# Performance work log

Hardware: AMD Instinct MI355X
Metric: run time of the kernel (lower is better)

## Reference

```python
import jax, jax.numpy as jnp
import numpy as np

N_CLASS = 85
BLANK = N_CLASS - 1  # blank_index = n_class - 1
ALPHA = 0.05
B, T, D = 4096, 96, 64


def setup_inputs() -> dict:
    key = jax.random.key(0)
    k1, k2, k3, k4 = jax.random.split(key, 4)
    preds = jax.random.normal(k1, (B, T, N_CLASS), dtype=jnp.float32)
    features = jax.random.normal(k2, (B, T, D), dtype=jnp.float32)
    labels = jax.random.randint(k3, (B, T), 0, N_CLASS, dtype=jnp.int32)
    centers = jax.random.normal(k4, (N_CLASS, D), dtype=jnp.float32) * 0.01
    return {"preds": preds, "features": features, "labels": labels, "centers": centers}


def _char_mask(pred_labels):
    # CTC collapse: keep non-blank positions that are the last of a repeat run.
    is_char = pred_labels != BLANK
    rep = pred_labels[:, :-1] == pred_labels[:, 1:]          # [B, T-1]
    tail = pred_labels[:, :1] > BLANK                         # always False (as in source)
    char_rep = jnp.concatenate([rep, tail], axis=1)           # [B, T]
    return is_char & jnp.logical_not(char_rep)


def reference(preds, features, labels, centers):
    # preds:    [B, T, n_class] softmax/logits -> argmax decode
    # features: [B, T, feat_dims]
    # labels:   [B, T] int, char label aligned to each timestep
    pred_labels = jnp.argmax(preds, axis=-1)                  # [B, T]
    mask = _char_mask(pred_labels).astype(features.dtype)     # [B, T] ragged-as-mask

    centers_batch = centers[labels]                           # gather -> [B, T, D]
    diff = centers_batch - features                           # [B, T, D]

    # tf.nn.l2_loss = sum(x^2)/2, restricted to valid char positions
    loss = 0.5 * jnp.sum(mask * jnp.sum(diff * diff, axis=-1))

    # unique_with_counts analog: per-class counts of valid char positions
    labels_flat = labels.reshape(-1)
    mask_flat = mask.reshape(-1)
    counts = jax.ops.segment_sum(mask_flat, labels_flat, num_segments=N_CLASS)  # [n_class]
    appear = counts[labels]                                   # [B, T]

    # alpha * diff / (1 + appear_times), zeroed outside char positions
    delta = ALPHA * diff * (mask / (1.0 + appear))[..., None]  # [B, T, D]

    # scatter_nd: centers.assign_sub(scatter of per-char deltas)
    upd = jax.ops.segment_sum(delta.reshape(-1, D), labels_flat, num_segments=N_CLASS)
    new_centers = centers - upd                               # [n_class, D]
    return loss, new_centers
```

## Files before the change

kernel.cpp:

```cpp
#include <hip/hip_runtime.h>
#include <cstdint>

#define BB     4096
#define TT     96
#define NC     85
#define BLANKC 84
#define DD     64
#define ALPHA  0.05f
#define BT     (BB * TT)
#define SLICE_F (NC * 17)
#define NF4    (TT * NC / 4)
#define RPBA   4
#define NBA    (BB / RPBA)
#define NBM    512

__global__ __launch_bounds__(512) void k_amask(const float4* __restrict__ p4,
                                               const int* __restrict__ labels,
                                               unsigned* __restrict__ labm,
                                               int* __restrict__ hpartT,
                                               float* __restrict__ out) {
    __shared__ float rows[8][12 * NC];
    __shared__ int   pls[RPBA * TT + 1];
    __shared__ int   h[NC];
    int tid  = threadIdx.x;
    int blk  = blockIdx.x;
    int lane = tid & 63;
    int w    = tid >> 6;
    if (tid < NC) h[tid] = 0;
    if (blk == 0 && tid == 480) out[0] = 0.f;
    int labreg = (tid < RPBA * TT) ? labels[blk * RPBA * TT + tid] : 0;

    const float4* src = p4 + (size_t)(blk * RPBA) * NF4 + 255 * w;
    float4 v0 = src[lane];
    float4 v1 = src[lane + 64];
    float4 v2 = src[lane + 128];
    float4 v3 = src[min(lane + 192, 254)];

    const int c0t[4] = {0, 22, 43, 64};
    const int c1t[4] = {22, 43, 64, 85};

    for (int i = 0; i < RPBA; ++i) {
        float4* dst = (float4*)rows[w];
        dst[lane]       = v0;
        dst[lane + 64]  = v1;
        dst[lane + 128] = v2;
        if (lane < 63) dst[lane + 192] = v3;
        if (i + 1 < RPBA) {
            const float4* s2 = p4 + (size_t)(blk * RPBA + i + 1) * NF4 + 255 * w;
            v0 = s2[lane];
            v1 = s2[lane + 64];
            v2 = s2[lane + 128];
            v3 = s2[min(lane + 192, 254)];
        }
        int r = lane >> 2, q = lane & 3;
        float bv = -3.4e38f; int bc = 127;
        if (lane < 48) {
            const float* row = rows[w] + r * NC;
            int c0 = c0t[q], c1 = c1t[q];
            bv = row[c0]; bc = c0;
            for (int c = c0 + 1; c < c1; ++c) {
                float v = row[c];
                if (v > bv) { bv = v; bc = c; }
            }
        }
#pragma unroll
        for (int m = 1; m <= 2; m <<= 1) {
            float ov = __shfl_xor(bv, m);
            int   oc = __shfl_xor(bc, m);
            if (ov > bv || (ov == bv && oc < bc)) { bv = ov; bc = oc; }
        }
        if (lane < 48 && (lane & 3) == 0) pls[i * TT + w * 12 + r] = bc;
    }
    __syncthreads();
    if (tid < RPBA * TT) {
        int p  = pls[tid];
        int lp = tid % TT;
        int m  = (p != BLANKC) && (lp == TT - 1 || p != pls[tid + 1]);
        labm[blk * RPBA * TT + tid] = (unsigned)labreg | ((unsigned)m << 31);
        atomicAdd(&h[labreg], m);
    }
    __syncthreads();
    if (tid < NC) hpartT[tid * NBA + blk] = h[tid];
}

__global__ __launch_bounds__(512, 6) void k_main(const float* __restrict__ feat,
                                                 const unsigned* __restrict__ labm,
                                                 float* __restrict__ updp,
                                                 float* __restrict__ lossp) {
    __shared__ float sl[8 * SLICE_F];
    __shared__ float lred[8];
    int tid = threadIdx.x;
    for (int i = tid; i < 8 * SLICE_F; i += 512) sl[i] = 0.f;
    __syncthreads();

    int lane = tid & 63;
    int w    = tid >> 6;
    int dq   = w & 3;
    int wg   = w >> 2;
    int sub  = lane >> 4;
    int l16  = lane & 15;
    float* slice = sl + w * SLICE_F;

    const int ppc = BT / (NBM * 2);
    const int nss = ppc / 16;
    int p0  = (blockIdx.x * 2 + wg) * ppc;
    const float* fbase = feat + dq * 16 + l16;

    float lsum = 0.f;
    float fA0, fA1, fA2, fA3, fB0, fB1, fB2, fB3;
    uint4 lA0, lA1, lA2, lA3, lB0, lB1, lB2, lB3;

#define ISSUE(P, f0, f1, f2, f3, q0, q1, q2, q3) do {            \
    int _p = (P);                                                \
    q0 = *(const uint4*)(labm + _p);                             \
    q1 = *(const uint4*)(labm + _p + 4);                         \
    q2 = *(const uint4*)(labm + _p + 8);                         \
    q3 = *(const uint4*)(labm + _p + 12);                        \
    f0 = fbase[(size_t)(_p + sub) * DD];                         \
    f1 = fbase[(size_t)(_p + 4 + sub) * DD];                     \
    f2 = fbase[(size_t)(_p + 8 + sub) * DD];                     \
    f3 = fbase[(size_t)(_p + 12 + sub) * DD];                    \
} while (0)

#define SUBSTEP(lv, fc) do {                                     \
    unsigned a0 = lv.x & 0x7fffffffu, a1 = lv.y & 0x7fffffffu,   \
             a2 = lv.z & 0x7fffffffu, a3 = lv.w & 0x7fffffffu;   \
    bool dup = (a0 == a1) | (a0 == a2) | (a0 == a3) |            \
               (a1 == a2) | (a1 == a3) | (a2 == a3);             \
    unsigned lw = (sub & 2) ? ((sub & 1) ? lv.w : lv.z)          \
                            : ((sub & 1) ? lv.y : lv.x);         \
    float m = (float)(lw >> 31);                                 \
    int  la = (int)(lw & 0x7fffffffu);                           \
    float c = m * (fc);                                          \
    lsum = fmaf(c, (fc), lsum);                                  \
    int a = la * 17 + l16;                                       \
    if (!dup) slice[a] += c;                                     \
    else      atomicAdd(&slice[a], c);                           \
} while (0)

    ISSUE(p0, fA0, fA1, fA2, fA3, lA0, lA1, lA2, lA3);
    for (int ss = 0; ss < nss; ss += 2) {
        if (ss + 1 < nss)
            ISSUE(p0 + (ss + 1) * 16, fB0, fB1, fB2, fB3, lB0, lB1, lB2, lB3);
        SUBSTEP(lA0, fA0); SUBSTEP(lA1, fA1);
        SUBSTEP(lA2, fA2); SUBSTEP(lA3, fA3);
        if (ss + 1 < nss) {
            if (ss + 2 < nss)
                ISSUE(p0 + (ss + 2) * 16, fA0, fA1, fA2, fA3, lA0, lA1, lA2, lA3);
            SUBSTEP(lB0, fB0); SUBSTEP(lB1, fB1);
            SUBSTEP(lB2, fB2); SUBSTEP(lB3, fB3);
        }
    }
#undef ISSUE
#undef SUBSTEP
    __syncthreads();

    float* myp = updp + (size_t)blockIdx.x * (NC * DD);
    for (int i = tid; i < NC * DD; i += 512) {
        int r = i >> 6, d = i & 63;
        int qq = d >> 4, d16 = d & 15;
        myp[i] = sl[qq * SLICE_F + r * 17 + d16] +
                 sl[(qq + 4) * SLICE_F + r * 17 + d16];
    }
#pragma unroll
    for (int off = 32; off; off >>= 1) lsum += __shfl_xor(lsum, off);
    if (lane == 0) lred[w] = lsum;
    __syncthreads();
    if (tid == 0) {
        float s = 0.f;
#pragma unroll
        for (int ww = 0; ww < 8; ++ww) s += lred[ww];
        lossp[blockIdx.x] = s;
    }
}

__global__ __launch_bounds__(256) void k_reduce(const float* __restrict__ updp,
                                                const float* __restrict__ lossp,
                                                const float* __restrict__ centers,
                                                const int* __restrict__ hpartT,
                                                float* __restrict__ out) {
    __shared__ float sred[256];
    __shared__ float sr[4];
    __shared__ int   scnt;
    int tid = threadIdx.x;
    int bid = blockIdx.x;
    if (bid < NC * 4) {
        int j = bid >> 2, q = bid & 3;
        int cs = 0;
        for (int t = tid; t < NBA; t += 256) cs += hpartT[j * NBA + t];
#pragma unroll
        for (int off = 32; off; off >>= 1) cs += __shfl_xor(cs, off);
        int lane = tid & 63, wv = tid >> 6;
        if (lane == 0) ((int*)sred)[wv] = cs;
        __syncthreads();
        if (tid == 0)
            scnt = ((int*)sred)[0] + ((int*)sred)[1] +
                   ((int*)sred)[2] + ((int*)sred)[3];
        __syncthreads();
        float cnt = (float)scnt;
        int i = tid & 15;
        int c16 = tid >> 4;
        const int per = NBM >> 4;
        int col = j * DD + q * 16 + i;
        float s = 0.f;
        for (int b = c16 * per; b < (c16 + 1) * per; ++b)
            s += updp[(size_t)b * (NC * DD) + col];
        sred[tid] = s;
        __syncthreads();
        if (tid < 16) {
            float F = 0.f;
#pragma unroll
            for (int cc = 0; cc < 16; ++cc) F += sred[cc * 16 + i];
            float c   = centers[col];
            float scale = ALPHA / (1.f + cnt);
            out[1 + col] = c - scale * (cnt * c - F);
            float lp = cnt * c * c - 2.f * c * F;
#pragma unroll
            for (int off = 8; off; off >>= 1) lp += __shfl_xor(lp, off);
            if (i == 0) atomicAdd(&out[0], 0.5f * lp);
        }
    } else {
        float s = 0.f;
        for (int t = tid; t < NBM; t += 256) s += lossp[t];
#pragma unroll
        for (int off = 32; off; off >>= 1) s += __shfl_xor(s, off);
        int lane = tid & 63, wv = tid >> 6;
        if (lane == 0) sr[wv] = s;
        __syncthreads();
        if (tid == 0) atomicAdd(&out[0], 0.5f * (sr[0] + sr[1] + sr[2] + sr[3]));
    }
}

extern "C" void kernel_launch(void* const* d_in, const int* in_sizes, int n_in,
                              void* d_out, int out_size, void* d_ws, size_t ws_size,
                              hipStream_t stream) {
    const float* preds    = (const float*)d_in[0];
    const float* features = (const float*)d_in[1];
    const int*   labels   = (const int*)d_in[2];
    const float* centers  = (const float*)d_in[3];
    float* out = (float*)d_out;

    char* ws = (char*)d_ws;
    unsigned* labm = (unsigned*)ws;
    int* hpartT    = (int*)(ws + 4 * (size_t)BT);
    size_t off0 = 4 * (size_t)BT + (size_t)NC * NBA * 4 + 512;
    float* lossp = (float*)(ws + off0);
    float* updp  = (float*)(ws + off0 + (size_t)NBM * 4 + 512);

    k_amask<<<NBA, 512, 0, stream>>>((const float4*)preds, labels, labm,
                                     hpartT, out);
    k_main<<<NBM, 512, 0, stream>>>(features, labm, updp, lossp);
    k_reduce<<<NC * 4 + 1, 256, 0, stream>>>(updp, lossp, centers, hpartT, out);
}
```

Baseline: 82.70 us.

## Precompute duplicate-label flags in mask kernel and widen main kernel to float2 per lane

The mask kernel now computes, for each group of four positions, whether any labels repeat, and stores that as bit 30 of the packed label word. The main kernel then reads this flag instead of doing six comparisons per substep. The main kernel is restructured to 256-thread blocks with 768 blocks, and each lane loads a float2 covering two feature dimensions, with wider shared-memory slices. The argmax loop is unrolled to a fixed 22-element span per quarter, with overlapping ranges and no lane guard. This trades more partial-update buffers for the reduce kernel against fewer instructions and wider loads in the hot loop.

```diff
diff --git a/kernel.cpp b/kernel.cpp
--- a/kernel.cpp
+++ b/kernel.cpp
@@ -8,11 +8,11 @@
 #define DD     64
 #define ALPHA  0.05f
 #define BT     (BB * TT)
-#define SLICE_F (NC * 17)
 #define NF4    (TT * NC / 4)
 #define RPBA   4
 #define NBA    (BB / RPBA)
-#define NBM    512
+#define NBM    768
+#define SL2    (NC * 34)
 
 __global__ __launch_bounds__(512) void k_amask(const float4* __restrict__ p4,
                                                const int* __restrict__ labels,
@@ -21,6 +21,7 @@
                                                float* __restrict__ out) {
     __shared__ float rows[8][12 * NC];
     __shared__ int   pls[RPBA * TT + 1];
+    __shared__ int   lab_s[RPBA * TT];
     __shared__ int   h[NC];
     int tid  = threadIdx.x;
     int blk  = blockIdx.x;
@@ -28,16 +29,17 @@
     int w    = tid >> 6;
     if (tid < NC) h[tid] = 0;
     if (blk == 0 && tid == 480) out[0] = 0.f;
-    int labreg = (tid < RPBA * TT) ? labels[blk * RPBA * TT + tid] : 0;
+    int labreg = 0;
+    if (tid < RPBA * TT) {
+        labreg = labels[blk * RPBA * TT + tid];
+        lab_s[tid] = labreg;
+    }
 
     const float4* src = p4 + (size_t)(blk * RPBA) * NF4 + 255 * w;
     float4 v0 = src[lane];
     float4 v1 = src[lane + 64];
     float4 v2 = src[lane + 128];
     float4 v3 = src[min(lane + 192, 254)];
-
-    const int c0t[4] = {0, 22, 43, 64};
-    const int c1t[4] = {22, 43, 64, 85};
 
     for (int i = 0; i < RPBA; ++i) {
         float4* dst = (float4*)rows[w];
@@ -53,15 +55,13 @@
             v3 = s2[min(lane + 192, 254)];
         }
         int r = lane >> 2, q = lane & 3;
-        float bv = -3.4e38f; int bc = 127;
-        if (lane < 48) {
-            const float* row = rows[w] + r * NC;
-            int c0 = c0t[q], c1 = c1t[q];
-            bv = row[c0]; bc = c0;
-            for (int c = c0 + 1; c < c1; ++c) {
-                float v = row[c];
-                if (v > bv) { bv = v; bc = c; }
-            }
+        int c0 = q * 21;
+        const float* row = rows[w] + (lane < 48 ? r : 0) * NC;
+        float bv = row[c0]; int bc = c0;
+#pragma unroll
+        for (int k = 1; k < 22; ++k) {
+            float v = row[c0 + k];
+            if (v > bv) { bv = v; bc = c0 + k; }
         }
 #pragma unroll
         for (int m = 1; m <= 2; m <<= 1) {
@@ -76,39 +76,45 @@
         int p  = pls[tid];
         int lp = tid % TT;
         int m  = (p != BLANKC) && (lp == TT - 1 || p != pls[tid + 1]);
-        labm[blk * RPBA * TT + tid] = (unsigned)labreg | ((unsigned)m << 31);
+        unsigned word = (unsigned)labreg | ((unsigned)m << 31);
+        int g = tid & ~3;
+        int l0 = lab_s[g], l1 = lab_s[g + 1], l2 = lab_s[g + 2], l3 = lab_s[g + 3];
+        bool dup = (l0 == l1) | (l0 == l2) | (l0 == l3) |
+                   (l1 == l2) | (l1 == l3) | (l2 == l3);
+        if ((tid & 3) == 0 && dup) word |= 0x40000000u;
+        labm[blk * RPBA * TT + tid] = word;
         atomicAdd(&h[labreg], m);
     }
     __syncthreads();
     if (tid < NC) hpartT[tid * NBA + blk] = h[tid];
 }
 
-__global__ __launch_bounds__(512, 6) void k_main(const float* __restrict__ feat,
+__global__ __launch_bounds__(256, 3) void k_main(const float* __restrict__ feat,
                                                  const unsigned* __restrict__ labm,
                                                  float* __restrict__ updp,
                                                  float* __restrict__ lossp) {
-    __shared__ float sl[8 * SLICE_F];
-    __shared__ float lred[8];
+    __shared__ float sl[4 * SL2];
+    __shared__ float lred[4];
     int tid = threadIdx.x;
-    for (int i = tid; i < 8 * SLICE_F; i += 512) sl[i] = 0.f;
+    for (int i = tid; i < 4 * SL2; i += 256) sl[i] = 0.f;
     __syncthreads();
 
     int lane = tid & 63;
     int w    = tid >> 6;
-    int dq   = w & 3;
-    int wg   = w >> 2;
+    int dimh = w & 1;
+    int wg   = w >> 1;
     int sub  = lane >> 4;
     int l16  = lane & 15;
-    float* slice = sl + w * SLICE_F;
+    float* slice = sl + w * SL2;
 
     const int ppc = BT / (NBM * 2);
     const int nss = ppc / 16;
-    int p0  = (blockIdx.x * 2 + wg) * ppc;
-    const float* fbase = feat + dq * 16 + l16;
+    int p0 = (blockIdx.x * 2 + wg) * ppc;
+    const float2* fb2 = (const float2*)feat + dimh * 16 + l16;
 
     float lsum = 0.f;
-    float fA0, fA1, fA2, fA3, fB0, fB1, fB2, fB3;
-    uint4 lA0, lA1, lA2, lA3, lB0, lB1, lB2, lB3;
+    float2 fA0, fA1, fA2, fA3, fB0, fB1, fB2, fB3;
+    uint4  lA0, lA1, lA2, lA3, lB0, lB1, lB2, lB3;
 
 #define ISSUE(P, f0, f1, f2, f3, q0, q1, q2, q3) do {            \
     int _p = (P);                                                \
@@ -116,26 +122,26 @@
     q1 = *(const uint4*)(labm + _p + 4);                         \
     q2 = *(const uint4*)(labm + _p + 8);                         \
     q3 = *(const uint4*)(labm + _p + 12);                        \
-    f0 = fbase[(size_t)(_p + sub) * DD];                         \
-    f1 = fbase[(size_t)(_p + 4 + sub) * DD];                     \
-    f2 = fbase[(size_t)(_p + 8 + sub) * DD];                     \
-    f3 = fbase[(size_t)(_p + 12 + sub) * DD];                    \
+    f0 = fb2[(size_t)(_p + sub) * 32];                           \
+    f1 = fb2[(size_t)(_p + 4 + sub) * 32];                       \
+    f2 = fb2[(size_t)(_p + 8 + sub) * 32];                       \
+    f3 = fb2[(size_t)(_p + 12 + sub) * 32];                      \
 } while (0)
 
 #define SUBSTEP(lv, fc) do {                                     \
-    unsigned a0 = lv.x & 0x7fffffffu, a1 = lv.y & 0x7fffffffu,   \
-             a2 = lv.z & 0x7fffffffu, a3 = lv.w & 0x7fffffffu;   \
-    bool dup = (a0 == a1) | (a0 == a2) | (a0 == a3) |            \
-               (a1 == a2) | (a1 == a3) | (a2 == a3);             \
     unsigned lw = (sub & 2) ? ((sub & 1) ? lv.w : lv.z)          \
                             : ((sub & 1) ? lv.y : lv.x);         \
-    float m = (float)(lw >> 31);                                 \
-    int  la = (int)(lw & 0x7fffffffu);                           \
-    float c = m * (fc);                                          \
-    lsum = fmaf(c, (fc), lsum);                                  \
-    int a = la * 17 + l16;                                       \
-    if (!dup) slice[a] += c;                                     \
-    else      atomicAdd(&slice[a], c);                           \
+    float m  = (float)(lw >> 31);                                \
+    int   la = (int)(lw & 0xffu);                                \
+    float cx = m * fc.x, cy = m * fc.y;                          \
+    lsum = fmaf(cx, fc.x, lsum);                                 \
+    lsum = fmaf(cy, fc.y, lsum);                                 \
+    int a = la * 34 + l16 * 2;                                   \
+    if (!((lv.x >> 30) & 1u)) {                                  \
+        slice[a] += cx; slice[a + 1] += cy;                      \
+    } else {                                                     \
+        atomicAdd(&slice[a], cx); atomicAdd(&slice[a + 1], cy);  \
+    }                                                            \
 } while (0)
 
     ISSUE(p0, fA0, fA1, fA2, fA3, lA0, lA1, lA2, lA3);
@@ -156,22 +162,18 @@
     __syncthreads();
 
     float* myp = updp + (size_t)blockIdx.x * (NC * DD);
-    for (int i = tid; i < NC * DD; i += 512) {
+    for (int i = tid; i < NC * DD; i += 256) {
         int r = i >> 6, d = i & 63;
-        int qq = d >> 4, d16 = d & 15;
-        myp[i] = sl[qq * SLICE_F + r * 17 + d16] +
-                 sl[(qq + 4) * SLICE_F + r * 17 + d16];
+        int dh = d >> 5, d32 = d & 31;
+        myp[i] = sl[dh * SL2 + r * 34 + d32] +
+                 sl[(2 + dh) * SL2 + r * 34 + d32];
     }
 #pragma unroll
     for (int off = 32; off; off >>= 1) lsum += __shfl_xor(lsum, off);
     if (lane == 0) lred[w] = lsum;
     __syncthreads();
-    if (tid == 0) {
-        float s = 0.f;
-#pragma unroll
-        for (int ww = 0; ww < 8; ++ww) s += lred[ww];
-        lossp[blockIdx.x] = s;
-    }
+    if (tid == 0)
+        lossp[blockIdx.x] = lred[0] + lred[1] + lred[2] + lred[3];
 }
 
 __global__ __launch_bounds__(256) void k_reduce(const float* __restrict__ updp,
@@ -249,6 +251,6 @@
 
     k_amask<<<NBA, 512, 0, stream>>>((const float4*)preds, labels, labm,
                                      hpartT, out);
-    k_main<<<NBM, 512, 0, stream>>>(features, labm, updp, lossp);
+    k_main<<<NBM, 256, 0, stream>>>(features, labm, updp, lossp);
     k_reduce<<<NC * 4 + 1, 256, 0, stream>>>(updp, lossp, centers, hpartT, out);
 }
```

After: 115.5 us. 39.7% more time.
